# Optimization experiments

Hardware: AMD Instinct MI355X
Metric: run time of the kernel (lower is better)

## Reference

```python
import jax, jax.numpy as jnp
from jax import lax
import numpy as np

VOCAB, EMB = 32000, 300
NF, FSIZES = 100, (3, 4, 5)
HID, OUT = 256, 32
B, T, L = 32, 64, 48


def setup_inputs() -> dict:
    key = jax.random.key(0)
    ks = jax.random.split(key, 16)
    inp = {}
    inp["dialogue"] = jax.random.randint(ks[0], (B, T, L), 0, VOCAB, dtype=jnp.int32)
    inp["emb"] = jax.random.normal(ks[1], (VOCAB, EMB), jnp.float32) * 0.1
    for j, fs in enumerate(FSIZES):
        inp[f"conv_w{fs}"] = jax.random.normal(ks[2 + j], (NF, EMB, fs), jnp.float32) * 0.05
        inp[f"conv_b{fs}"] = jnp.zeros((NF,), jnp.float32)
    D = NF * len(FSIZES)  # LSTM input size = 300
    for j, tag in enumerate(("f", "r")):
        inp[f"w_ih_{tag}"] = jax.random.normal(ks[5 + 2 * j], (4 * HID, D), jnp.float32) * 0.05
        inp[f"w_hh_{tag}"] = jax.random.normal(ks[6 + 2 * j], (4 * HID, HID), jnp.float32) * 0.05
        inp[f"b_ih_{tag}"] = jnp.zeros((4 * HID,), jnp.float32)
        inp[f"b_hh_{tag}"] = jnp.zeros((4 * HID,), jnp.float32)
    inp["head_w"] = jax.random.normal(ks[9], (OUT, 2 * HID), jnp.float32) * 0.05
    inp["head_b"] = jnp.zeros((OUT,), jnp.float32)
    return inp


def _lstm(x_tbd, w_ih, w_hh, b_ih, b_hh):
    # x_tbd: [T, B, D] -> hidden sequence [T, B, H]; torch gate order i,f,g,o
    H = w_hh.shape[1]
    Bsz = x_tbd.shape[1]
    # precompute input projections for all timesteps in one GEMM
    xg = jnp.einsum('tbd,gd->tbg', x_tbd, w_ih) + (b_ih + b_hh)

    def step(carry, xg_t):
        h, c = carry
        gates = xg_t + h @ w_hh.T
        i, f, g, o = jnp.split(gates, 4, axis=-1)
        c = jax.nn.sigmoid(f) * c + jax.nn.sigmoid(i) * jnp.tanh(g)
        h = jax.nn.sigmoid(o) * jnp.tanh(c)
        return (h, c), h

    h0 = jnp.zeros((Bsz, H), x_tbd.dtype)
    _, hs = lax.scan(step, (h0, h0), xg)
    return hs


def reference(dialogue, emb, conv_w3, conv_b3, conv_w4, conv_b4, conv_w5, conv_b5,
              w_ih_f, w_hh_f, b_ih_f, b_hh_f, w_ih_r, w_hh_r, b_ih_r, b_hh_r,
              head_w, head_b):
    Bd, Td, Ld = dialogue.shape
    x = emb[dialogue.reshape(Bd * Td, Ld)]      # [BT, L, E]
    x = x.transpose(0, 2, 1)                     # [BT, E, L] (NCH)
    feats = []
    for w, b in ((conv_w3, conv_b3), (conv_w4, conv_b4), (conv_w5, conv_b5)):
        # Conv2d(1,NF,(fs,E)) on [BT,1,L,E] == 1D valid conv over L with E in-channels
        y = lax.conv_general_dilated(x, w, (1,), 'VALID',
                                     dimension_numbers=('NCH', 'OIH', 'NCH'))
        y = jax.nn.relu(y + b[None, :, None])    # [BT, NF, L-fs+1]
        feats.append(jnp.max(y, axis=2))         # max_pool1d over full width
    r_in = jnp.concatenate(feats, axis=1).reshape(Bd, Td, -1)  # dropout = identity (eval)
    xt = r_in.transpose(1, 0, 2)                 # [T, B, D]
    hf = _lstm(xt, w_ih_f, w_hh_f, b_ih_f, b_hh_f)            # forward direction
    hr = _lstm(xt[::-1], w_ih_r, w_hh_r, b_ih_r, b_hh_r)[::-1]  # reverse direction
    h = jnp.concatenate([hf, hr], axis=-1).transpose(1, 0, 2)  # [B, T, 2H]
    return jax.nn.sigmoid(jnp.einsum('bth,oh->bto', h, head_w) + head_b)
```

## Files before the change

kernel.cpp:

```cpp
#include <hip/hip_runtime.h>
#include <math.h>

typedef unsigned short u16;
typedef unsigned int   u32;
typedef unsigned long long u64;
typedef float  v16f __attribute__((ext_vector_type(16)));
typedef short  v8s  __attribute__((ext_vector_type(8)));
typedef unsigned int v4u __attribute__((ext_vector_type(4)));

__device__ __forceinline__ float sigf(float x) { return 1.0f / (1.0f + __expf(-x)); }
__device__ __forceinline__ float tanhfast(float x) { return 2.0f / (1.0f + __expf(-2.0f * x)) - 1.0f; }
__device__ __forceinline__ u16 f2bf(float f) {
    u32 x = __float_as_uint(f);
    u32 r = (x + 0x7fffu + ((x >> 16) & 1u)) >> 16;
    return (u16)r;
}

#define LD3SYS(v0, v1, v2, p0, p1, p2)                                        \
    asm volatile("global_load_dwordx4 %0, %3, off sc1\n\t"                    \
                 "global_load_dwordx4 %1, %4, off sc1\n\t"                    \
                 "global_load_dwordx4 %2, %5, off sc1\n\t"                    \
                 "s_waitcnt vmcnt(0)"                                         \
                 : "=&v"(v0), "=&v"(v1), "=&v"(v2)                            \
                 : "v"(p0), "v"(p1), "v"(p2)                                  \
                 : "memory")

#define ST16SYS(p, v)                                                         \
    asm volatile("global_store_dwordx4 %0, %1, off sc1"                       \
                 :: "v"(p), "v"(v) : "memory")

#define KE        19
#define SLAB      2048
#define G0_OFF    0
#define G1_OFF    (3 * KE * SLAB)
#define G2_OFF    (7 * KE * SLAB)
#define WKR_TOT   (12 * KE * SLAB)
#define XSTR      312

__global__ __launch_bounds__(256) void k_cprep(const float* __restrict__ w3,
                                               const float* __restrict__ w4,
                                               const float* __restrict__ w5,
                                               u16* __restrict__ wkr) {
    const int gid = blockIdx.x * 256 + threadIdx.x;
    int g, rem;
    if (gid < G1_OFF)      { g = 0; rem = gid; }
    else if (gid < G2_OFF) { g = 1; rem = gid - G1_OFF; }
    else                   { g = 2; rem = gid - G2_OFF; }
    const int fs = 3 + g;
    const int j  = rem & 7;
    const int q  = (rem >> 3) & 1;
    const int f  = (rem >> 4) & 127;
    const int t  = rem >> 11;
    const int ke = t % KE;
    const int kk = t / KE;
    const int e  = ke * 16 + q * 8 + j;
    float v = 0.0f;
    if (f < 100 && e < 300) {
        const float* w = (g == 0) ? w3 : (g == 1) ? w4 : w5;
        v = w[((size_t)f * 300 + e) * fs + kk];
    }
    wkr[gid] = f2bf(v);
}

__global__ __launch_bounds__(384) void k_conv_mfma(const int* __restrict__ dlg,
                                                   const float* __restrict__ emb,
                                                   const u16* __restrict__ wkr,
                                                   const float* __restrict__ b3,
                                                   const float* __restrict__ b4,
                                                   const float* __restrict__ b5,
                                                   float* __restrict__ feat) {
    __shared__ u16 xT[104 * XSTR];
    __shared__ int toks[96];
    const int u2  = blockIdx.x;
    const int tid = threadIdx.x;
    if (tid < 96) toks[tid] = dlg[u2 * 96 + tid];
    __syncthreads();
    for (int i = tid; i < 96 * 75; i += 384) {
        int t  = i / 75;
        int e4 = i - t * 75;
        int utt = (t >= 48);
        int row = utt * 52 + (t - utt * 48);
        float4 v = *(const float4*)(emb + (size_t)toks[t] * 300 + e4 * 4);
        uint2 o;
        o.x = (u32)f2bf(v.x) | ((u32)f2bf(v.y) << 16);
        o.y = (u32)f2bf(v.z) | ((u32)f2bf(v.w) << 16);
        *(uint2*)&xT[row * XSTR + e4 * 4] = o;
    }
    for (int i = tid; i < 8 * (XSTR / 2); i += 384) {
        int r = i / (XSTR / 2);
        int c = i - r * (XSTR / 2);
        int row = (r < 4) ? (48 + r) : (96 + r - 4);
        *(u32*)&xT[row * XSTR + c * 2] = 0;
    }
    __syncthreads();

    const int wv   = tid >> 6;
    const int lane = tid & 63;
    const int m    = lane & 31;
    const int q    = lane >> 5;

    int abase[3];
#pragma unroll
    for (int mt = 0; mt < 3; ++mt) {
        int r = mt * 32 + m;
        int utt = (r >= 48);
        int p = r - utt * 48;
        abase[mt] = (utt * 52 + p) * XSTR + q * 8;
    }

    int gA, ntA, gB, ntB, kkA, kkB;
    if (wv < 4) { gA = 0; ntA = wv; gB = 2; ntB = wv; kkA = 3; kkB = 5; }
    else        { gA = 1; ntA = (wv - 4) * 2; gB = 1; ntB = ntA + 1; kkA = 4; kkB = 4; }
    const int goffA = (gA == 0) ? G0_OFF : (gA == 1) ? G1_OFF : G2_OFF;
    const int goffB = (gB == 0) ? G0_OFF : (gB == 1) ? G1_OFF : G2_OFF;
    const u16* wA = wkr + goffA + ((ntA * 32 + m) * 2 + q) * 8;
    const u16* wB = wkr + goffB + ((ntB * 32 + m) * 2 + q) * 8;

    v16f accA[3], accB[3];
#pragma unroll
    for (int mt = 0; mt < 3; ++mt) {
#pragma unroll
        for (int r = 0; r < 16; ++r) { accA[mt][r] = 0.0f; accB[mt][r] = 0.0f; }
    }

    const int kmin = (kkA < kkB) ? kkA : kkB;
    const u16* pA = wA;
    const u16* pB = wB;
    v8s bfA = *(const v8s*)pA;
    v8s bfB = *(const v8s*)pB;
    for (int kk = 0; kk < kmin; ++kk) {
        const int xshift = kk * XSTR;
        for (int ke = 0; ke < KE; ++ke) {
            v8s cA = bfA, cB = bfB;
            pA += SLAB; pB += SLAB;
            bfA = *(const v8s*)pA;
            bfB = *(const v8s*)pB;
            const int xcol = xshift + ke * 16;
#pragma unroll
            for (int mt = 0; mt < 3; ++mt) {
                v8s af = *(const v8s*)&xT[abase[mt] + xcol];
                accA[mt] = __builtin_amdgcn_mfma_f32_32x32x16_bf16(af, cA, accA[mt], 0, 0, 0);
                accB[mt] = __builtin_amdgcn_mfma_f32_32x32x16_bf16(af, cB, accB[mt], 0, 0, 0);
            }
        }
    }
    for (int kk = kmin; kk < kkB; ++kk) {
        const int xshift = kk * XSTR;
        for (int ke = 0; ke < KE; ++ke) {
            v8s cB = bfB;
            pB += SLAB;
            bfB = *(const v8s*)pB;
            const int xcol = xshift + ke * 16;
#pragma unroll
            for (int mt = 0; mt < 3; ++mt) {
                v8s af = *(const v8s*)&xT[abase[mt] + xcol];
                accB[mt] = __builtin_amdgcn_mfma_f32_32x32x16_bf16(af, cB, accB[mt], 0, 0, 0);
            }
        }
    }

    const int PP[3] = {46, 45, 44};
#pragma unroll
    for (int which = 0; which < 2; ++which) {
        const int g  = which ? gB : gA;
        const int nt = which ? ntB : ntA;
        const v16f* acc = which ? accB : accA;
        const float* bg = (g == 0) ? b3 : (g == 1) ? b4 : b5;
        const int f = nt * 32 + m;
        const float bias = (f < 100) ? bg[f] : 0.0f;
        const int Pg = PP[g];
        float v0 = -1e30f, v1 = -1e30f;
#pragma unroll
        for (int mt = 0; mt < 3; ++mt) {
#pragma unroll
            for (int reg = 0; reg < 16; ++reg) {
                int row = (reg & 3) + 8 * (reg >> 2) + 4 * q;
                int r = mt * 32 + row;
                int utt = (r >= 48);
                int p = r - utt * 48;
                if (p < Pg) {
                    float val = acc[mt][reg] + bias;
                    if (utt) v1 = fmaxf(v1, val); else v0 = fmaxf(v0, val);
                }
            }
        }
        v0 = fmaxf(v0, __shfl_xor(v0, 32, 64));
        v1 = fmaxf(v1, __shfl_xor(v1, 32, 64));
        if (q == 0 && f < 100) {
            feat[((size_t)(u2 * 2 + 0)) * 300 + g * 100 + f] = fmaxf(0.0f, v0);
            feat[((size_t)(u2 * 2 + 1)) * 300 + g * 100 + f] = fmaxf(0.0f, v1);
        }
    }
}

__global__ __launch_bounds__(256) void k_xg(const float* __restrict__ feat,
                                            const float* __restrict__ wih_f, const float* __restrict__ bih_f,
                                            const float* __restrict__ bhh_f,
                                            const float* __restrict__ wih_r, const float* __restrict__ bih_r,
                                            const float* __restrict__ bhh_r,
                                            float* __restrict__ xgF) {
    __shared__ float fls[300 * 36];
    const int bx  = blockIdx.x;
    const int dir = bx >> 8;
    const int t   = (bx >> 2) & 63;
    const int gc  = bx & 3;
    const int tid = threadIdx.x;
    for (int i = tid; i < 32 * 300; i += 256) {
        int b = i / 300;
        int d = i - b * 300;
        fls[d * 36 + b] = feat[((size_t)b * 64 + t) * 300 + d];
    }
    __syncthreads();
    const int g = gc * 256 + tid;
    const float* wih = dir ? wih_r : wih_f;
    const float* bih = dir ? bih_r : bih_f;
    const float* bhh = dir ? bhh_r : bhh_f;
    const float* wr  = wih + (size_t)g * 300;
    const float bias = bih[g] + bhh[g];
    float acc[32];
#pragma unroll
    for (int b = 0; b < 32; ++b) acc[b] = 0.0f;
    for (int d = 0; d < 300; d += 4) {
        float4 wv = *(const float4*)(wr + d);
#pragma unroll
        for (int j = 0; j < 4; ++j) {
            float w = (j == 0) ? wv.x : (j == 1) ? wv.y : (j == 2) ? wv.z : wv.w;
            const float* r = &fls[(d + j) * 36];
#pragma unroll
            for (int bq = 0; bq < 8; ++bq) {
                float4 x = *(const float4*)(r + bq * 4);
                acc[bq * 4 + 0] = fmaf(w, x.x, acc[bq * 4 + 0]);
                acc[bq * 4 + 1] = fmaf(w, x.y, acc[bq * 4 + 1]);
                acc[bq * 4 + 2] = fmaf(w, x.z, acc[bq * 4 + 2]);
                acc[bq * 4 + 3] = fmaf(w, x.w, acc[bq * 4 + 3]);
            }
        }
    }
    const int jj      = tid;
    const int js      = jj >> 6;
    const int n_local = ((jj & 63) << 2) | gc;
    const int nt      = n_local >> 5;
    const int lane_lo = n_local & 31;
    float* base = xgF + (((size_t)(dir * 64 + t) * 32) + js * 8 + nt) * 1024;
#pragma unroll
    for (int b = 0; b < 32; ++b) {
        int q    = (b >> 2) & 1;
        int reg  = (b & 3) + ((b >> 3) << 2);
        base[reg * 64 + lane_lo + (q << 5)] = acc[b] + bias;
    }
}

__global__ __launch_bounds__(256) void k_prep3(const float* __restrict__ whh_f,
                                               const float* __restrict__ whh_r,
                                               u16* __restrict__ wpk3) {
    const int gid  = blockIdx.x * 256 + threadIdx.x;
    const int j    = gid & 7;
    const int lane = (gid >> 3) & 63;
    const int kt   = (gid >> 9) & 15;
    const int nt   = (gid >> 13) & 7;
    const int js   = (gid >> 16) & 3;
    const int dir  = (gid >> 18) & 1;
    const int n_local = nt * 32 + (lane & 31);
    const int jjl  = n_local >> 2;
    const int gate = n_local & 3;
    const int k    = kt * 16 + (lane >> 5) * 8 + j;
    const int row  = gate * 256 + js * 64 + jjl;
    const float* whh = dir ? whh_r : whh_f;
    wpk3[gid] = f2bf(whh[(size_t)row * 256 + k]);
}

__global__ __launch_bounds__(256) void k_init(v4u* __restrict__ hxrec) {
    const int id = blockIdx.x * 256 + threadIdx.x;
    v4u z; z[0] = 0u; z[1] = 0u; z[2] = 0u; z[3] = 0u;
    hxrec[id] = z;
}

__global__ __launch_bounds__(512) void k_lstm3(const u16* __restrict__ wpk3,
                                               const float* __restrict__ xgF,
                                               u32* __restrict__ hxrec,
                                               float* __restrict__ hseq) {
    __shared__ u32   hbuf[32 * 132];
    __shared__ float gbuf[32 * 276];
    const int dir = blockIdx.x >> 2;
    const int js  = blockIdx.x & 3;
    const int tid = threadIdx.x;
    const int w   = tid >> 6;
    const int l   = tid & 63;
    const int m   = l & 31;
    const int q   = l >> 5;

    v8s Bf[16];
    {
        const u16* wb = wpk3 + ((((size_t)dir * 4 + js) * 8 + w) * 16) * 512 + (size_t)l * 8;
#pragma unroll
        for (int kt = 0; kt < 16; ++kt) Bf[kt] = *(const v8s*)(wb + kt * 512);
    }

    const int eb  = tid & 31;
    const int ejb = tid >> 5;
    float cst[4], hval[4];
#pragma unroll
    for (int c2 = 0; c2 < 4; ++c2) { cst[c2] = 0.0f; hval[c2] = 0.0f; }

    float* hout = hseq + (size_t)dir * 64 * 32 * 256;
    u32* hx_d   = hxrec + (size_t)dir * 2 * 2048 * 4;
    const u32* hx0 = hx_d;
    const u32* hx1 = hx_d + 2048 * 4;

    int roff[3], hoff[3];
#pragma unroll
    for (int i = 0; i < 3; ++i) {
        int flat = i * 512 + tid;
        int b    = flat / 48;
        int r    = flat - b * 48;
        int q64  = r + (r >= js * 16 ? 16 : 0);
        roff[i]  = (b * 64 + q64) * 4;
        hoff[i]  = b * 132 + q64 * 2;
    }
    const int woff = (eb * 64 + js * 16 + ejb) * 4;

    for (int s = 0; s < 64; ++s) {
        const int t = dir ? (63 - s) : s;
        v16f acc;
        const float* xb = xgF + (((size_t)(dir * 64 + t) * 32) + js * 8 + w) * 1024 + l;
#pragma unroll
        for (int r = 0; r < 16; ++r) acc[r] = xb[r * 64];

        if (s > 0) {
            const u32* hxs = (s & 1) ? hx1 : hx0;
            const u32* p0 = hxs + roff[0];
            const u32* p1 = hxs + roff[1];
            const u32* p2 = hxs + roff[2];
            v4u v0, v1, v2;
            LD3SYS(v0, v1, v2, p0, p1, p2);
            const u32 ts = (u32)s;
            u32 guard = 0;
            while (v0[2] != ts || v1[2] != ts || v2[2] != ts) {
                if (++guard > (1u << 22)) break;
                LD3SYS(v0, v1, v2, p0, p1, p2);
            }
            *(u64*)&hbuf[hoff[0]] = (u64)v0[0] | ((u64)v0[1] << 32);
            *(u64*)&hbuf[hoff[1]] = (u64)v1[0] | ((u64)v1[1] << 32);
            *(u64*)&hbuf[hoff[2]] = (u64)v2[0] | ((u64)v2[1] << 32);
        } else {
            for (int i = tid; i < 32 * 132; i += 512) hbuf[i] = 0u;
        }
        {
            u64 pk = (u64)f2bf(hval[0]) | ((u64)f2bf(hval[1]) << 16)
                   | ((u64)f2bf(hval[2]) << 32) | ((u64)f2bf(hval[3]) << 48);
            *(u64*)&hbuf[eb * 132 + (js * 16 + ejb) * 2] = pk;
        }
        __syncthreads();

#pragma unroll
        for (int kt = 0; kt < 16; ++kt) {
            v8s af = *(const v8s*)&hbuf[m * 132 + kt * 8 + q * 4];
            acc = __builtin_amdgcn_mfma_f32_32x32x16_bf16(af, Bf[kt], acc, 0, 0, 0);
        }

#pragma unroll
        for (int r = 0; r < 16; ++r) {
            int row = (r & 3) + 8 * (r >> 2) + 4 * q;
            gbuf[row * 276 + w * 32 + m] = acc[r];
        }
        __syncthreads();

        {
            const float* gb = &gbuf[eb * 276 + ejb * 16];
#pragma unroll
            for (int c2 = 0; c2 < 4; ++c2) {
                float4 gv = *(const float4*)(gb + c2 * 4);
                float i_ = sigf(gv.x), f_ = sigf(gv.y);
                float g_ = tanhfast(gv.z), o_ = sigf(gv.w);
                cst[c2] = f_ * cst[c2] + i_ * g_;
                hval[c2] = o_ * tanhfast(cst[c2]);
            }
        }
        {
            float4 hv4 = make_float4(hval[0], hval[1], hval[2], hval[3]);
            *(float4*)&hout[((size_t)t * 32 + eb) * 256 + js * 64 + ejb * 4] = hv4;
            u64 pk = (u64)f2bf(hval[0]) | ((u64)f2bf(hval[1]) << 16)
                   | ((u64)f2bf(hval[2]) << 32) | ((u64)f2bf(hval[3]) << 48);
            v4u rec;
            rec[0] = (u32)pk;
            rec[1] = (u32)(pk >> 32);
            rec[2] = (u32)(s + 1);
            rec[3] = 0u;
            u32* pw = (u32*)(((s & 1) ? hx0 : hx1) + woff);
            ST16SYS(pw, rec);
        }
    }
}

__global__ __launch_bounds__(256) void k_head(const float* __restrict__ hseq,
                                              const float* __restrict__ hw,
                                              const float* __restrict__ hb,
                                              float* __restrict__ out) {
    const int id = blockIdx.x * 256 + threadIdx.x;
    const int o  = id & 31;
    const int u  = id >> 5;
    const int b  = u >> 6, t = u & 63;
    const float* pf = hseq + ((size_t)t * 32 + b) * 256;
    const float* pr = hseq + (size_t)64 * 32 * 256 + ((size_t)t * 32 + b) * 256;
    const float* wo = hw + (size_t)o * 512;
    float acc = hb[o];
    for (int j = 0; j < 256; j += 4) {
        float4 wa = *(const float4*)(wo + j);
        float4 wb = *(const float4*)(wo + 256 + j);
        float4 fa = *(const float4*)(pf + j);
        float4 fb = *(const float4*)(pr + j);
        acc = fmaf(wa.x, fa.x, acc); acc = fmaf(wa.y, fa.y, acc);
        acc = fmaf(wa.z, fa.z, acc); acc = fmaf(wa.w, fa.w, acc);
        acc = fmaf(wb.x, fb.x, acc); acc = fmaf(wb.y, fb.y, acc);
        acc = fmaf(wb.z, fb.z, acc); acc = fmaf(wb.w, fb.w, acc);
    }
    out[id] = sigf(acc);
}

extern "C" void kernel_launch(void* const* d_in, const int* in_sizes, int n_in,
                              void* d_out, int out_size, void* d_ws, size_t ws_size,
                              hipStream_t stream) {
    const int*   dlg   = (const int*)d_in[0];
    const float* emb   = (const float*)d_in[1];
    const float* w3    = (const float*)d_in[2];  const float* b3    = (const float*)d_in[3];
    const float* w4    = (const float*)d_in[4];  const float* b4    = (const float*)d_in[5];
    const float* w5    = (const float*)d_in[6];  const float* b5    = (const float*)d_in[7];
    const float* wih_f = (const float*)d_in[8];  const float* whh_f = (const float*)d_in[9];
    const float* bih_f = (const float*)d_in[10]; const float* bhh_f = (const float*)d_in[11];
    const float* wih_r = (const float*)d_in[12]; const float* whh_r = (const float*)d_in[13];
    const float* bih_r = (const float*)d_in[14]; const float* bhh_r = (const float*)d_in[15];
    const float* hw    = (const float*)d_in[16]; const float* hb    = (const float*)d_in[17];
    float* out = (float*)d_out;

    float* f     = (float*)d_ws;
    float* feat  = f;
    float* xgF   = f + 614400;
    float* hseq  = f + 4808704;
    u16*   wkr   = (u16*)(f + 5857280);
    u16*   wpk3  = (u16*)(f + 6090752);
    u32*   hxrec = (u32*)(f + 6352896);

    hipLaunchKernelGGL(k_init, dim3(32), dim3(256), 0, stream, (v4u*)hxrec);
    hipLaunchKernelGGL(k_cprep, dim3(WKR_TOT / 256), dim3(256), 0, stream,
                       w3, w4, w5, wkr);
    hipLaunchKernelGGL(k_prep3, dim3(2048), dim3(256), 0, stream,
                       whh_f, whh_r, wpk3);
    hipLaunchKernelGGL(k_conv_mfma, dim3(1024), dim3(384), 0, stream,
                       dlg, emb, wkr, b3, b4, b5, feat);
    hipLaunchKernelGGL(k_xg, dim3(512), dim3(256), 0, stream,
                       feat, wih_f, bih_f, bhh_f, wih_r, bih_r, bhh_r, xgF);
    hipLaunchKernelGGL(k_lstm3, dim3(8), dim3(512), 0, stream,
                       wpk3, xgF, hxrec, hseq);
    hipLaunchKernelGGL(k_head, dim3(256), dim3(256), 0, stream,
                       hseq, hw, hb, out);
}
```

Baseline: 558.6 us.

## Halve LSTM recurrence blocks per direction, doubling hidden slice per block

Each LSTM direction now runs on 2 workgroups instead of 4. Every wave holds two B-fragment sets and issues two MFMA chains per step. The gate nonlinearity is done in two phases through the shared gate buffer, which adds extra barriers. The aim is to cut cross-workgroup global-memory handshake traffic and polling latency per timestep (2 loads instead of 3 per thread), at the cost of twice the per-block MFMA and elementwise work plus higher register pressure.

```diff
diff --git a/kernel.cpp b/kernel.cpp
--- a/kernel.cpp
+++ b/kernel.cpp
@@ -16,13 +16,12 @@
     return (u16)r;
 }
 
-#define LD3SYS(v0, v1, v2, p0, p1, p2)                                        \
-    asm volatile("global_load_dwordx4 %0, %3, off sc1\n\t"                    \
-                 "global_load_dwordx4 %1, %4, off sc1\n\t"                    \
-                 "global_load_dwordx4 %2, %5, off sc1\n\t"                    \
+#define LD2SYS(v0, v1, p0, p1)                                                \
+    asm volatile("global_load_dwordx4 %0, %2, off sc1\n\t"                    \
+                 "global_load_dwordx4 %1, %3, off sc1\n\t"                    \
                  "s_waitcnt vmcnt(0)"                                         \
-                 : "=&v"(v0), "=&v"(v1), "=&v"(v2)                            \
-                 : "v"(p0), "v"(p1), "v"(p2)                                  \
+                 : "=&v"(v0), "=&v"(v1)                                       \
+                 : "v"(p0), "v"(p1)                                           \
                  : "memory")
 
 #define ST16SYS(p, v)                                                         \
@@ -281,90 +280,105 @@
                                                float* __restrict__ hseq) {
     __shared__ u32   hbuf[32 * 132];
     __shared__ float gbuf[32 * 276];
-    const int dir = blockIdx.x >> 2;
-    const int js  = blockIdx.x & 3;
+    const int dir = blockIdx.x >> 1;
+    const int jh  = blockIdx.x & 1;
     const int tid = threadIdx.x;
     const int w   = tid >> 6;
     const int l   = tid & 63;
     const int m   = l & 31;
     const int q   = l >> 5;
 
-    v8s Bf[16];
+    const int sub = w >> 2;
+    const int jsw = jh * 2 + sub;
+    const int nt0 = w & 3;
+    const int nt1 = (w & 3) + 4;
+
+    v8s Bf0[16], Bf1[16];
     {
-        const u16* wb = wpk3 + ((((size_t)dir * 4 + js) * 8 + w) * 16) * 512 + (size_t)l * 8;
-#pragma unroll
-        for (int kt = 0; kt < 16; ++kt) Bf[kt] = *(const v8s*)(wb + kt * 512);
+        const u16* wb0 = wpk3 + ((((size_t)dir * 4 + jsw) * 8 + nt0) * 16) * 512 + (size_t)l * 8;
+        const u16* wb1 = wpk3 + ((((size_t)dir * 4 + jsw) * 8 + nt1) * 16) * 512 + (size_t)l * 8;
+#pragma unroll
+        for (int kt = 0; kt < 16; ++kt) {
+            Bf0[kt] = *(const v8s*)(wb0 + kt * 512);
+            Bf1[kt] = *(const v8s*)(wb1 + kt * 512);
+        }
     }
 
     const int eb  = tid & 31;
     const int ejb = tid >> 5;
-    float cst[4], hval[4];
-#pragma unroll
-    for (int c2 = 0; c2 < 4; ++c2) { cst[c2] = 0.0f; hval[c2] = 0.0f; }
+    float cst[8], hval[8];
+#pragma unroll
+    for (int c2 = 0; c2 < 8; ++c2) { cst[c2] = 0.0f; hval[c2] = 0.0f; }
 
     float* hout = hseq + (size_t)dir * 64 * 32 * 256;
     u32* hx_d   = hxrec + (size_t)dir * 2 * 2048 * 4;
     const u32* hx0 = hx_d;
     const u32* hx1 = hx_d + 2048 * 4;
 
-    int roff[3], hoff[3];
-#pragma unroll
-    for (int i = 0; i < 3; ++i) {
+    int roff[2], hoff[2];
+#pragma unroll
+    for (int i = 0; i < 2; ++i) {
         int flat = i * 512 + tid;
-        int b    = flat / 48;
-        int r    = flat - b * 48;
-        int q64  = r + (r >= js * 16 ? 16 : 0);
+        int b    = flat >> 5;
+        int r    = flat & 31;
+        int q64  = (1 - jh) * 32 + r;
         roff[i]  = (b * 64 + q64) * 4;
         hoff[i]  = b * 132 + q64 * 2;
     }
-    const int woff = (eb * 64 + js * 16 + ejb) * 4;
+    const int woff0 = (eb * 64 + jh * 32 + ejb) * 4;
+    const int woff1 = (eb * 64 + jh * 32 + 16 + ejb) * 4;
 
     for (int s = 0; s < 64; ++s) {
         const int t = dir ? (63 - s) : s;
-        v16f acc;
-        const float* xb = xgF + (((size_t)(dir * 64 + t) * 32) + js * 8 + w) * 1024 + l;
-#pragma unroll
-        for (int r = 0; r < 16; ++r) acc[r] = xb[r * 64];
+        v16f acc0, acc1;
+        const float* xb0 = xgF + (((size_t)(dir * 64 + t) * 32) + jsw * 8 + nt0) * 1024 + l;
+        const float* xb1 = xgF + (((size_t)(dir * 64 + t) * 32) + jsw * 8 + nt1) * 1024 + l;
+#pragma unroll
+        for (int r = 0; r < 16; ++r) { acc0[r] = xb0[r * 64]; acc1[r] = xb1[r * 64]; }
 
         if (s > 0) {
             const u32* hxs = (s & 1) ? hx1 : hx0;
             const u32* p0 = hxs + roff[0];
             const u32* p1 = hxs + roff[1];
-            const u32* p2 = hxs + roff[2];
-            v4u v0, v1, v2;
-            LD3SYS(v0, v1, v2, p0, p1, p2);
+            v4u v0, v1;
+            LD2SYS(v0, v1, p0, p1);
             const u32 ts = (u32)s;
             u32 guard = 0;
-            while (v0[2] != ts || v1[2] != ts || v2[2] != ts) {
+            while (v0[2] != ts || v1[2] != ts) {
                 if (++guard > (1u << 22)) break;
-                LD3SYS(v0, v1, v2, p0, p1, p2);
+                LD2SYS(v0, v1, p0, p1);
             }
             *(u64*)&hbuf[hoff[0]] = (u64)v0[0] | ((u64)v0[1] << 32);
             *(u64*)&hbuf[hoff[1]] = (u64)v1[0] | ((u64)v1[1] << 32);
-            *(u64*)&hbuf[hoff[2]] = (u64)v2[0] | ((u64)v2[1] << 32);
         } else {
             for (int i = tid; i < 32 * 132; i += 512) hbuf[i] = 0u;
         }
         {
-            u64 pk = (u64)f2bf(hval[0]) | ((u64)f2bf(hval[1]) << 16)
-                   | ((u64)f2bf(hval[2]) << 32) | ((u64)f2bf(hval[3]) << 48);
-            *(u64*)&hbuf[eb * 132 + (js * 16 + ejb) * 2] = pk;
+            u64 pk0 = (u64)f2bf(hval[0]) | ((u64)f2bf(hval[1]) << 16)
+                    | ((u64)f2bf(hval[2]) << 32) | ((u64)f2bf(hval[3]) << 48);
+            u64 pk1 = (u64)f2bf(hval[4]) | ((u64)f2bf(hval[5]) << 16)
+                    | ((u64)f2bf(hval[6]) << 32) | ((u64)f2bf(hval[7]) << 48);
+            *(u64*)&hbuf[eb * 132 + (jh * 32 + ejb) * 2] = pk0;
+            *(u64*)&hbuf[eb * 132 + (jh * 32 + 16 + ejb) * 2] = pk1;
         }
         __syncthreads();
 
 #pragma unroll
         for (int kt = 0; kt < 16; ++kt) {
             v8s af = *(const v8s*)&hbuf[m * 132 + kt * 8 + q * 4];
-            acc = __builtin_amdgcn_mfma_f32_32x32x16_bf16(af, Bf[kt], acc, 0, 0, 0);
-        }
-
-#pragma unroll
-        for (int r = 0; r < 16; ++r) {
-            int row = (r & 3) + 8 * (r >> 2) + 4 * q;
-            gbuf[row * 276 + w * 32 + m] = acc[r];
+            acc0 = __builtin_amdgcn_mfma_f32_32x32x16_bf16(af, Bf0[kt], acc0, 0, 0, 0);
+            acc1 = __builtin_amdgcn_mfma_f32_32x32x16_bf16(af, Bf1[kt], acc1, 0, 0, 0);
+        }
+
+        if (sub == 0) {
+#pragma unroll
+            for (int r = 0; r < 16; ++r) {
+                int row = (r & 3) + 8 * (r >> 2) + 4 * q;
+                gbuf[row * 276 + nt0 * 32 + m] = acc0[r];
+                gbuf[row * 276 + nt1 * 32 + m] = acc1[r];
+            }
         }
         __syncthreads();
-
         {
             const float* gb = &gbuf[eb * 276 + ejb * 16];
 #pragma unroll
@@ -376,18 +390,45 @@
                 hval[c2] = o_ * tanhfast(cst[c2]);
             }
         }
+        __syncthreads();
+        if (sub == 1) {
+#pragma unroll
+            for (int r = 0; r < 16; ++r) {
+                int row = (r & 3) + 8 * (r >> 2) + 4 * q;
+                gbuf[row * 276 + nt0 * 32 + m] = acc0[r];
+                gbuf[row * 276 + nt1 * 32 + m] = acc1[r];
+            }
+        }
+        __syncthreads();
         {
-            float4 hv4 = make_float4(hval[0], hval[1], hval[2], hval[3]);
-            *(float4*)&hout[((size_t)t * 32 + eb) * 256 + js * 64 + ejb * 4] = hv4;
-            u64 pk = (u64)f2bf(hval[0]) | ((u64)f2bf(hval[1]) << 16)
-                   | ((u64)f2bf(hval[2]) << 32) | ((u64)f2bf(hval[3]) << 48);
-            v4u rec;
-            rec[0] = (u32)pk;
-            rec[1] = (u32)(pk >> 32);
-            rec[2] = (u32)(s + 1);
-            rec[3] = 0u;
-            u32* pw = (u32*)(((s & 1) ? hx0 : hx1) + woff);
-            ST16SYS(pw, rec);
+            const float* gb = &gbuf[eb * 276 + ejb * 16];
+#pragma unroll
+            for (int c2 = 0; c2 < 4; ++c2) {
+                float4 gv = *(const float4*)(gb + c2 * 4);
+                float i_ = sigf(gv.x), f_ = sigf(gv.y);
+                float g_ = tanhfast(gv.z), o_ = sigf(gv.w);
+                cst[4 + c2] = f_ * cst[4 + c2] + i_ * g_;
+                hval[4 + c2] = o_ * tanhfast(cst[4 + c2]);
+            }
+        }
+
+        {
+            float4 hvA = make_float4(hval[0], hval[1], hval[2], hval[3]);
+            float4 hvB = make_float4(hval[4], hval[5], hval[6], hval[7]);
+            float* ho = &hout[((size_t)t * 32 + eb) * 256];
+            *(float4*)&ho[(2 * jh) * 64 + ejb * 4]     = hvA;
+            *(float4*)&ho[(2 * jh + 1) * 64 + ejb * 4] = hvB;
+            u64 pk0 = (u64)f2bf(hval[0]) | ((u64)f2bf(hval[1]) << 16)
+                    | ((u64)f2bf(hval[2]) << 32) | ((u64)f2bf(hval[3]) << 48);
+            u64 pk1 = (u64)f2bf(hval[4]) | ((u64)f2bf(hval[5]) << 16)
+                    | ((u64)f2bf(hval[6]) << 32) | ((u64)f2bf(hval[7]) << 48);
+            v4u rec0, rec1;
+            rec0[0] = (u32)pk0; rec0[1] = (u32)(pk0 >> 32); rec0[2] = (u32)(s + 1); rec0[3] = 0u;
+            rec1[0] = (u32)pk1; rec1[1] = (u32)(pk1 >> 32); rec1[2] = (u32)(s + 1); rec1[3] = 0u;
+            u32* pw0 = (u32*)(((s & 1) ? hx0 : hx1) + woff0);
+            u32* pw1 = (u32*)(((s & 1) ? hx0 : hx1) + woff1);
+            ST16SYS(pw0, rec0);
+            ST16SYS(pw1, rec1);
         }
     }
 }
@@ -449,7 +490,7 @@
                        dlg, emb, wkr, b3, b4, b5, feat);
     hipLaunchKernelGGL(k_xg, dim3(512), dim3(256), 0, stream,
                        feat, wih_f, bih_f, bhh_f, wih_r, bih_r, bhh_r, xgF);
-    hipLaunchKernelGGL(k_lstm3, dim3(8), dim3(512), 0, stream,
+    hipLaunchKernelGGL(k_lstm3, dim3(4), dim3(512), 0, stream,
                        wpk3, xgF, hxrec, hseq);
     hipLaunchKernelGGL(k_head, dim3(256), dim3(256), 0, stream,
                        hseq, hw, hb, out);
```

Result: slower. 719.1 us (+28.7%).

## Localize LSTM gate math per warp and prefetch next-step input projections

Applied to the files above, without the earlier changes.

Each wavefront now stages its own MFMA gate results into a private shared-memory slab and computes the cell update for the hidden units it produced. This removes the block-wide barrier between the gate GEMM and the elementwise update. The next timestep's xg values are loaded into registers one step ahead to hide global latency. The cross-block hidden-state record is published before the hseq store, shortening the critical path of the recurrence, at the cost of more registers (af, xcur arrays) and a different ownership mapping.

```diff
diff --git a/kernel.cpp b/kernel.cpp
--- a/kernel.cpp
+++ b/kernel.cpp
@@ -280,7 +280,7 @@
                                                u32* __restrict__ hxrec,
                                                float* __restrict__ hseq) {
     __shared__ u32   hbuf[32 * 132];
-    __shared__ float gbuf[32 * 276];
+    __shared__ float slab[8 * 32 * 36];
     const int dir = blockIdx.x >> 2;
     const int js  = blockIdx.x & 3;
     const int tid = threadIdx.x;
@@ -296,11 +296,11 @@
         for (int kt = 0; kt < 16; ++kt) Bf[kt] = *(const v8s*)(wb + kt * 512);
     }
 
-    const int eb  = tid & 31;
-    const int ejb = tid >> 5;
+    const int jp = l & 1;
+    const int bl = l >> 1;
     float cst[4], hval[4];
 #pragma unroll
-    for (int c2 = 0; c2 < 4; ++c2) { cst[c2] = 0.0f; hval[c2] = 0.0f; }
+    for (int c = 0; c < 4; ++c) { cst[c] = 0.0f; hval[c] = 0.0f; }
 
     float* hout = hseq + (size_t)dir * 64 * 32 * 256;
     u32* hx_d   = hxrec + (size_t)dir * 2 * 2048 * 4;
@@ -317,16 +317,34 @@
         roff[i]  = (b * 64 + q64) * 4;
         hoff[i]  = b * 132 + q64 * 2;
     }
-    const int woff = (eb * 64 + js * 16 + ejb) * 4;
+    const int woff = (bl * 64 + js * 16 + 2 * w + jp) * 4;
+    const int hown = bl * 132 + (js * 16 + 2 * w + jp) * 2;
+
+    float* sl = &slab[w * 32 * 36];
+
+    float xcur[16];
+    {
+        const int t0 = dir ? 63 : 0;
+        const float* xb = xgF + (((size_t)(dir * 64 + t0) * 32) + js * 8 + w) * 1024 + l;
+#pragma unroll
+        for (int r = 0; r < 16; ++r) xcur[r] = xb[r * 64];
+    }
 
     for (int s = 0; s < 64; ++s) {
-        const int t = dir ? (63 - s) : s;
         v16f acc;
-        const float* xb = xgF + (((size_t)(dir * 64 + t) * 32) + js * 8 + w) * 1024 + l;
-#pragma unroll
-        for (int r = 0; r < 16; ++r) acc[r] = xb[r * 64];
+#pragma unroll
+        for (int r = 0; r < 16; ++r) acc[r] = xcur[r];
+        if (s < 63) {
+            const int tn = dir ? (62 - s) : (s + 1);
+            const float* xb = xgF + (((size_t)(dir * 64 + tn) * 32) + js * 8 + w) * 1024 + l;
+#pragma unroll
+            for (int r = 0; r < 16; ++r) xcur[r] = xb[r * 64];
+        }
 
         if (s > 0) {
+            u64 pk = (u64)f2bf(hval[0]) | ((u64)f2bf(hval[1]) << 16)
+                   | ((u64)f2bf(hval[2]) << 32) | ((u64)f2bf(hval[3]) << 48);
+            *(u64*)&hbuf[hown] = pk;
             const u32* hxs = (s & 1) ? hx1 : hx0;
             const u32* p0 = hxs + roff[0];
             const u32* p1 = hxs + roff[1];
@@ -345,40 +363,34 @@
         } else {
             for (int i = tid; i < 32 * 132; i += 512) hbuf[i] = 0u;
         }
-        {
-            u64 pk = (u64)f2bf(hval[0]) | ((u64)f2bf(hval[1]) << 16)
-                   | ((u64)f2bf(hval[2]) << 32) | ((u64)f2bf(hval[3]) << 48);
-            *(u64*)&hbuf[eb * 132 + (js * 16 + ejb) * 2] = pk;
-        }
         __syncthreads();
 
-#pragma unroll
-        for (int kt = 0; kt < 16; ++kt) {
-            v8s af = *(const v8s*)&hbuf[m * 132 + kt * 8 + q * 4];
-            acc = __builtin_amdgcn_mfma_f32_32x32x16_bf16(af, Bf[kt], acc, 0, 0, 0);
-        }
+        v8s af[16];
+#pragma unroll
+        for (int kt = 0; kt < 16; ++kt)
+            af[kt] = *(const v8s*)&hbuf[m * 132 + kt * 8 + q * 4];
+        __syncthreads();
+
+#pragma unroll
+        for (int kt = 0; kt < 16; ++kt)
+            acc = __builtin_amdgcn_mfma_f32_32x32x16_bf16(af[kt], Bf[kt], acc, 0, 0, 0);
 
 #pragma unroll
         for (int r = 0; r < 16; ++r) {
             int row = (r & 3) + 8 * (r >> 2) + 4 * q;
-            gbuf[row * 276 + w * 32 + m] = acc[r];
-        }
-        __syncthreads();
+            sl[row * 36 + m] = acc[r];
+        }
+#pragma unroll
+        for (int c = 0; c < 4; ++c) {
+            float4 gv = *(const float4*)&sl[bl * 36 + jp * 16 + c * 4];
+            float i_ = sigf(gv.x), f_ = sigf(gv.y);
+            float g_ = tanhfast(gv.z), o_ = sigf(gv.w);
+            cst[c]  = f_ * cst[c] + i_ * g_;
+            hval[c] = o_ * tanhfast(cst[c]);
+        }
 
         {
-            const float* gb = &gbuf[eb * 276 + ejb * 16];
-#pragma unroll
-            for (int c2 = 0; c2 < 4; ++c2) {
-                float4 gv = *(const float4*)(gb + c2 * 4);
-                float i_ = sigf(gv.x), f_ = sigf(gv.y);
-                float g_ = tanhfast(gv.z), o_ = sigf(gv.w);
-                cst[c2] = f_ * cst[c2] + i_ * g_;
-                hval[c2] = o_ * tanhfast(cst[c2]);
-            }
-        }
-        {
-            float4 hv4 = make_float4(hval[0], hval[1], hval[2], hval[3]);
-            *(float4*)&hout[((size_t)t * 32 + eb) * 256 + js * 64 + ejb * 4] = hv4;
+            const int t = dir ? (63 - s) : s;
             u64 pk = (u64)f2bf(hval[0]) | ((u64)f2bf(hval[1]) << 16)
                    | ((u64)f2bf(hval[2]) << 32) | ((u64)f2bf(hval[3]) << 48);
             v4u rec;
@@ -388,6 +400,8 @@
             rec[3] = 0u;
             u32* pw = (u32*)(((s & 1) ? hx0 : hx1) + woff);
             ST16SYS(pw, rec);
+            float4 hv4 = make_float4(hval[0], hval[1], hval[2], hval[3]);
+            *(float4*)&hout[((size_t)t * 32 + bl) * 256 + js * 64 + 8 * w + 4 * jp] = hv4;
         }
     }
 }
```

Measured after the change: 550.2 us. No clear change (-1.5%).
